# Kernel optimization log

Measured on AMD Instinct MI355X. Metric: run time of the kernel, lower is better.

Reference implementation:

```python
import jax, jax.numpy as jnp
import numpy as np

C = 128                  # stem_dim
CONV_DIM = C * C * 3 * 3 # 147456
B, T = 32, 30
N_CH = 1024
N_ANS = 32               # n_answers + 1
V = 44

UNARY = [4,10,11,12,13,14,15,16,17,18,19,20,21,22,23,24,25,29,30,31,32,33,34,35,36,37,38,39,40,41,43]
BINARY = [5,6,7,8,9,26,27,28,42]
SCENE_TOK = 4

_kind = np.zeros(V, np.int32)   # 0=special, 1=scene, 2=unary, 3=binary
_uidx = np.zeros(V, np.int32)
_bidx = np.zeros(V, np.int32)
for _j, _t in enumerate(UNARY):
    _kind[_t] = 2; _uidx[_t] = _j
for _j, _t in enumerate(BINARY):
    _kind[_t] = 3; _bidx[_t] = _j
_kind[SCENE_TOK] = 1
KIND_T, U_T, B_T = jnp.array(_kind), jnp.array(_uidx), jnp.array(_bidx)


def conv3x3(x, w):  # x [N,C,H,W], w [O,I,3,3], pad=1
    return jax.lax.conv_general_dilated(x, w, (1, 1), ((1, 1), (1, 1)),
                                        dimension_numbers=('NCHW', 'OIHW', 'NCHW'))


def conv1x1(x, w):
    return jax.lax.conv_general_dilated(x, w, (1, 1), ((0, 0), (0, 0)),
                                        dimension_numbers=('NCHW', 'OIHW', 'NCHW'))

# per-sample weights: vmap conv over batch
_bconv = jax.vmap(lambda x, w: conv3x3(x[None], w)[0])


def exec_unary(x, w1, w2):
    return jax.nn.relu(_bconv(jax.nn.relu(_bconv(x, w1)), w2))


def exec_binary(x1, x2, w1, w2, w3):
    h = jax.nn.relu(_bconv(jnp.concatenate([x1, x2], axis=1), w1))
    h = jax.nn.relu(_bconv(h, w2))
    return jax.nn.relu(_bconv(h, w3))


def setup_inputs() -> dict:
    key = jax.random.key(0)
    ks = jax.random.split(key, 10)
    std = 1.0 / float(np.sqrt(CONV_DIM))
    r = lambda k, shp, s: jax.random.normal(k, shp, jnp.float32) * s
    return {
        'feats': jax.random.normal(ks[0], (B, N_CH, 14, 14), jnp.float32),
        'programs': jax.random.randint(ks[1], (B, T), 0, V, dtype=jnp.int32),
        'stem_w1': r(ks[2], (C, N_CH, 3, 3), 0.02),
        'stem_b1': jnp.zeros((C,), jnp.float32),
        'stem_w2': r(ks[3], (C, C, 3, 3), 0.05),
        'stem_b2': jnp.zeros((C,), jnp.float32),
        'mem_u': jax.random.uniform(ks[4], (31, 2 * CONV_DIM), jnp.float32, -std, std),
        'mem_b': jax.random.uniform(ks[5], (9, 4 * CONV_DIM), jnp.float32, -std, std),
        'cls_w': r(ks[6], (512, C, 1, 1), 0.05),
        'cls_b': jnp.zeros((512,), jnp.float32),
        'fc1_w': r(ks[7], (1024, 512 * 7 * 7), 0.01),
        'fc1_b': jnp.zeros((1024,), jnp.float32),
        'fc2_w': r(ks[8], (N_ANS, 1024), 0.03),
        'fc2_b': jnp.zeros((N_ANS,), jnp.float32),
    }


def reference(feats, programs, stem_w1, stem_b1, stem_w2, stem_b2, mem_u, mem_b,
              cls_w, cls_b, fc1_w, fc1_b, fc2_w, fc2_b):
    # stem: conv3x3 -> relu -> conv3x3 -> relu
    h = jax.nn.relu(conv3x3(feats, stem_w1) + stem_b1[None, :, None, None])
    feat = jax.nn.relu(conv3x3(h, stem_w2) + stem_b2[None, :, None, None])  # [B,C,14,14]

    def step(carry, tok):  # tok [B] int32
        out, saved = carry
        kind = KIND_T[tok]                           # [B]
        uread = mem_u[U_T[tok]]                      # [B, 2*CONV_DIM] one-hot memory read
        w1 = uread[:, :CONV_DIM].reshape(-1, C, C, 3, 3)
        w2 = uread[:, CONV_DIM:].reshape(-1, C, C, 3, 3)
        bread = mem_b[B_T[tok]]                      # [B, 4*CONV_DIM]
        bw1 = bread[:, :2 * CONV_DIM].reshape(-1, C, 2 * C, 3, 3)
        bw2 = bread[:, 2 * CONV_DIM:3 * CONV_DIM].reshape(-1, C, C, 3, 3)
        bw3 = bread[:, 3 * CONV_DIM:].reshape(-1, C, C, 3, 3)
        is_scene = (kind == 1)[:, None, None, None]
        u_in = jnp.where(is_scene, feat, out)        # scene runs on stem features
        u_out = exec_unary(u_in, w1, w2)
        b_out = exec_binary(out, saved, bw1, bw2, bw3)
        k4 = kind[:, None, None, None]
        new_saved = jnp.where(is_scene, out, saved)  # scene saves current output
        new_out = jnp.where(k4 == 0, out, jnp.where(k4 == 3, b_out, u_out))
        return (new_out, new_saved), None

    toks_rev = programs[:, ::-1].T.astype(jnp.int32)  # [T,B] reversed program
    (out, _), _ = jax.lax.scan(step, (feat, jnp.zeros_like(feat)), toks_rev)

    # classifier: conv1x1 -> relu -> maxpool2 -> flatten -> fc -> relu -> fc
    h = jax.nn.relu(conv1x1(out, cls_w) + cls_b[None, :, None, None])
    h = jax.lax.reduce_window(h, -jnp.inf, jax.lax.max, (1, 1, 2, 2), (1, 1, 2, 2), 'VALID')
    h = h.reshape(h.shape[0], -1)                     # [B, 512*7*7]
    h = jax.nn.relu(h @ fc1_w.T + fc1_b)
    return h @ fc2_w.T + fc2_b                        # [B, N_ANS]
```

## Files before the change

### kernel.cpp

```cpp
#include <hip/hip_runtime.h>


#define NSTEP 30
#define CD 147456
#define P 196
#define FSZ 25088
#define LROW 18
#define LBUF (272*LROW)

typedef __attribute__((ext_vector_type(8))) short short8;
typedef __attribute__((ext_vector_type(16))) float f32x16;

__constant__ int KIND_TBL[44] = {
  0,0,0,0,1,3,3,3,3,3, 2,2,2,2,2,2,2,2,2,2,
  2,2,2,2,2,2,3,3,3,2, 2,2,2,2,2,2,2,2,2,2, 2,2,3,2};
__constant__ int MIDX_TBL[44] = {
  0,0,0,0,0,0,1,2,3,4, 1,2,3,4,5,6,7,8,9,10,
  11,12,13,14,15,16,5,6,7,17, 18,19,20,21,22,23,24,25,26,27, 28,29,8,30};

__device__ __forceinline__ uint32_t bf16_rne(float x) {
  uint32_t u = __float_as_uint(x);
  return (u + 0x7fffu + ((u >> 16) & 1u)) >> 16;
}
__device__ __forceinline__ uint32_t pack_hl(float x) {
  uint32_t h = bf16_rne(x);
  float rest = x - __uint_as_float(h << 16);
  uint32_t l = bf16_rne(rest);
  return (h << 16) | l;
}
__device__ __forceinline__ float ld_sc0(const float* p) {
  return __hip_atomic_load(p, __ATOMIC_RELAXED, __HIP_MEMORY_SCOPE_AGENT);
}
__device__ __forceinline__ void st_sc(float* p, float v) {
  __hip_atomic_store(p, v, __ATOMIC_RELAXED, __HIP_MEMORY_SCOPE_AGENT);
}

__device__ __forceinline__ void bbar(int* __restrict__ ctr, int target) {
  __syncthreads();
  if (threadIdx.x == 0) {
    __hip_atomic_fetch_add(ctr, 1, __ATOMIC_RELAXED, __HIP_MEMORY_SCOPE_AGENT);
    while (__hip_atomic_load(ctr, __ATOMIC_RELAXED, __HIP_MEMORY_SCOPE_AGENT) < target)
      __builtin_amdgcn_s_sleep(2);
  }
  __syncthreads();
}

__global__ void __launch_bounds__(256) repack_kernel(
    const float* __restrict__ sw1, const float* __restrict__ sw2,
    const float* __restrict__ mu, const float* __restrict__ mb,
    uint32_t* __restrict__ Wp)
{
  const int blk = blockIdx.x;
  const int C = blk / 9, tap = blk % 9;
  const float* src; int nic, lc;
  if (C < 64)       { src = sw1; nic = 1024; lc = C; }
  else if (C < 72)  { src = sw2; nic = 128;  lc = C - 64; }
  else if (C < 568) { int u = (C - 72) >> 4, r = (C - 72) & 15;
                      src = mu + (size_t)u * 2 * CD + (size_t)(r >> 3) * CD;
                      nic = 128; lc = r & 7; }
  else              { int j = (C - 568) >> 5, r = (C - 568) & 31;
                      const float* base = mb + (size_t)j * 4 * CD;
                      if (r < 16)      { src = base;                  nic = 256; lc = r; }
                      else if (r < 24) { src = base + 2 * (size_t)CD; nic = 128; lc = r - 16; }
                      else             { src = base + 3 * (size_t)CD; nic = 128; lc = r - 24; } }
  const int mt = threadIdx.x >> 6, lane = threadIdx.x & 63;
  const int oc = mt * 32 + (lane & 31);
  const int ic0 = lc * 16 + (lane >> 5) * 8;
  uint32_t hw[4], lw[4];
#pragma unroll
  for (int pr = 0; pr < 4; ++pr) {
    uint32_t hh[2], ll[2];
#pragma unroll
    for (int e = 0; e < 2; ++e) {
      float x = src[((size_t)oc * nic + (ic0 + pr * 2 + e)) * 9 + tap];
      uint32_t h = bf16_rne(x);
      float rest = x - __uint_as_float(h << 16);
      hh[e] = h; ll[e] = bf16_rne(rest);
    }
    hw[pr] = hh[0] | (hh[1] << 16);
    lw[pr] = ll[0] | (ll[1] << 16);
  }
  uint32_t* dstb = Wp + (size_t)blk * 2048;
  *(uint4*)(dstb + (mt * 2 + 0) * 256 + lane * 4) = make_uint4(hw[0], hw[1], hw[2], hw[3]);
  *(uint4*)(dstb + (mt * 2 + 1) * 256 + lane * 4) = make_uint4(lw[0], lw[1], lw[2], lw[3]);
}

union BU { uint32_t u[4]; uint4 v; short8 s8; };

__device__ __forceinline__ void load_wchunk(const uint32_t* __restrict__ wb,
                                            BU* wh, BU* wl) {
#pragma unroll
  for (int t = 0; t < 9; ++t) {
    wh[t].v = *(const uint4*)(wb + t * 2048);
    wl[t].v = *(const uint4*)(wb + t * 2048 + 256);
  }
}

__device__ __forceinline__ void mfma_chunk(const uint32_t* __restrict__ sb,
                                           int pwbase, const BU* wh, const BU* wl,
                                           f32x16& acc) {
  const int TAPOFF[9] = {0, 1, 2, 16, 17, 18, 32, 33, 34};
#pragma unroll
  for (int tap = 0; tap < 9; ++tap) {
    const int pw = pwbase + TAPOFF[tap] * LROW;
    uint2 q0 = *(const uint2*)(sb + pw);
    uint2 q1 = *(const uint2*)(sb + pw + 2);
    uint2 q2 = *(const uint2*)(sb + pw + 4);
    uint2 q3 = *(const uint2*)(sb + pw + 6);
    BU Bh, Bl;
    Bh.u[0] = __builtin_amdgcn_perm(q0.y, q0.x, 0x07060302u);
    Bh.u[1] = __builtin_amdgcn_perm(q1.y, q1.x, 0x07060302u);
    Bh.u[2] = __builtin_amdgcn_perm(q2.y, q2.x, 0x07060302u);
    Bh.u[3] = __builtin_amdgcn_perm(q3.y, q3.x, 0x07060302u);
    Bl.u[0] = __builtin_amdgcn_perm(q0.y, q0.x, 0x05040100u);
    Bl.u[1] = __builtin_amdgcn_perm(q1.y, q1.x, 0x05040100u);
    Bl.u[2] = __builtin_amdgcn_perm(q2.y, q2.x, 0x05040100u);
    Bl.u[3] = __builtin_amdgcn_perm(q3.y, q3.x, 0x05040100u);
    acc = __builtin_amdgcn_mfma_f32_32x32x16_bf16(wh[tap].s8, Bh.s8, acc, 0, 0, 0);
    acc = __builtin_amdgcn_mfma_f32_32x32x16_bf16(wh[tap].s8, Bl.s8, acc, 0, 0, 0);
    acc = __builtin_amdgcn_mfma_f32_32x32x16_bf16(wl[tap].s8, Bh.s8, acc, 0, 0, 0);
  }
}

template<int MODE>
__device__ __forceinline__ void stage_load(
    const float* __restrict__ in0A, const float* __restrict__ in0B,
    const float* __restrict__ in1A, const float* __restrict__ in1B,
    int split, int cn, int ic16, const int* imgoff, float* sv)
{
  if (MODE == 0) {
    const float* sA = in0A + (size_t)(cn * 16 + ic16) * P;
#pragma unroll
    for (int i = 0; i < 9; ++i) {
      int off = imgoff[i];
      sv[i] = (off >= 0) ? sA[off] : 0.f;
    }
  } else if (MODE == 1) {
    size_t o = (size_t)(cn * 16 + ic16) * P;
    const float* sA = in0A + o;
    const float* sB = in0B + o;
#pragma unroll
    for (int i = 0; i < 9; ++i) {
      int off = imgoff[i];
      sv[i] = (off >= 0) ? fmaxf(ld_sc0(sA + off) + ld_sc0(sB + off), 0.f) : 0.f;
    }
  } else {
    const float* sA; const float* sB;
    if (cn < split) {
      size_t o = (size_t)(cn * 16 + ic16) * P;
      sA = in0A + o; sB = in0B + o;
    } else {
      size_t o = (size_t)((cn - split) * 16 + ic16) * P;
      sA = in1A + o; sB = in1B + o;
    }
#pragma unroll
    for (int i = 0; i < 9; ++i) {
      int off = imgoff[i];
      sv[i] = (off >= 0) ? fmaxf(ld_sc0(sA + off) + ld_sc0(sB + off), 0.f) : 0.f;
    }
  }
}

template<int MODE>
__device__ __forceinline__ void conv_run(
    uint32_t sbuf[2][LBUF],
    const float* __restrict__ in0A, const float* __restrict__ in0B,
    const float* __restrict__ in1A, const float* __restrict__ in1B,
    int split, int cbeg, int n,
    int C0, int mt,
    const uint32_t* __restrict__ Wp, const float* __restrict__ bias,
    float* __restrict__ dst, float* __restrict__ dst2, float* __restrict__ zb,
    const int* imgoff)
{
  const int tid = threadIdx.x;
  const int w = tid >> 6, lane = tid & 63, l31 = lane & 31, kq = lane >> 5;
  const int ic16 = tid >> 5, pl = tid & 31;
  const int pwbase = (32 * w + l31) * LROW + kq * 8;
  const bool cw = (w < 7);
  const uint32_t* wbase = Wp + (size_t)C0 * 9 * 2048 + (mt * 2) * 256 + lane * 4;

  f32x16 acc;
#pragma unroll
  for (int i = 0; i < 16; ++i) acc[i] = 0.f;

  BU whA[9], wlA[9], whB[9], wlB[9];
  if (cw) load_wchunk(wbase + (size_t)cbeg * 9 * 2048, whA, wlA);
  {
    float sv[9];
    stage_load<MODE>(in0A, in0B, in1A, in1B, split, cbeg, ic16, imgoff, sv);
#pragma unroll
    for (int i = 0; i < 9; ++i) {
      int p = pl + 32 * i;
      if (p < 272) sbuf[0][p * LROW + ic16] = pack_hl(sv[i]);
    }
  }
  __syncthreads();

  int k = 0;
  while (true) {
    {
      const bool more = (k + 1 < n);
      float sv[9];
      if (more) {
        stage_load<MODE>(in0A, in0B, in1A, in1B, split, cbeg + k + 1, ic16, imgoff, sv);
        if (cw) load_wchunk(wbase + (size_t)(cbeg + k + 1) * 9 * 2048, whB, wlB);
      }
      if (cw) mfma_chunk(&sbuf[k & 1][0], pwbase, whA, wlA, acc);
      if (more) {
#pragma unroll
        for (int i = 0; i < 9; ++i) {
          int p = pl + 32 * i;
          if (p < 272) sbuf[(k + 1) & 1][p * LROW + ic16] = pack_hl(sv[i]);
        }
      }
      __syncthreads();
      if (++k >= n) break;
    }
    {
      const bool more = (k + 1 < n);
      float sv[9];
      if (more) {
        stage_load<MODE>(in0A, in0B, in1A, in1B, split, cbeg + k + 1, ic16, imgoff, sv);
        if (cw) load_wchunk(wbase + (size_t)(cbeg + k + 1) * 9 * 2048, whA, wlA);
      }
      if (cw) mfma_chunk(&sbuf[k & 1][0], pwbase, whB, wlB, acc);
      if (more) {
#pragma unroll
        for (int i = 0; i < 9; ++i) {
          int p = pl + 32 * i;
          if (p < 272) sbuf[(k + 1) & 1][p * LROW + ic16] = pack_hl(sv[i]);
        }
      }
      __syncthreads();
      if (++k >= n) break;
    }
  }

  if (cw) {
    const int ox = l31 & 15, oy = 2 * w + (l31 >> 4);
    if (ox < 14) {
#pragma unroll
      for (int reg = 0; reg < 16; ++reg) {
        int row = (reg & 3) + 8 * (reg >> 2) + 4 * kq;
        int oc = mt * 32 + row;
        float v = acc[reg];
        if (bias) v += bias[row];
        st_sc(dst + (size_t)oc * P + oy * 14 + ox, v);
        if (dst2) st_sc(dst2 + (size_t)oc * P + oy * 14 + ox, v);
        if (zb)   st_sc(zb   + (size_t)oc * P + oy * 14 + ox, 0.f);
      }
    }
  }
}

__global__ void __launch_bounds__(512, 1) persist_kernel(
    const float* __restrict__ feats, const int* __restrict__ progs,
    const float* __restrict__ sb1, const float* __restrict__ sb2,
    const uint32_t* __restrict__ Wp,
    float* __restrict__ featA, float* __restrict__ featB,
    float* __restrict__ outbA, float* __restrict__ outbB,
    float* __restrict__ savedA, float* __restrict__ savedB,
    float* __restrict__ h1A, float* __restrict__ h1B,
    float* __restrict__ h2A, float* __restrict__ h2B,
    int* __restrict__ ctr)
{
  __shared__ uint32_t s_act[2][LBUF];
  const int tid = threadIdx.x;
  const int b = blockIdx.x & 31;
  const int slice = blockIdx.x >> 5;
  const int mt = slice & 3;
  const int kh = slice >> 2;
  const size_t bo = (size_t)b * FSZ;
  int* myctr = ctr + b * 32;
  int phase = 0;

  float* featP  = kh ? featB  : featA;
  float* outbP  = kh ? outbB  : outbA;
  float* savedP = kh ? savedB : savedA;
  float* h1P    = kh ? h1B    : h1A;
  float* h2P    = kh ? h2B    : h2A;
  const float* bias1 = kh ? nullptr : sb1 + mt * 32;
  const float* bias2 = kh ? nullptr : sb2 + mt * 32;

  int imgoff[9];
#pragma unroll
  for (int i = 0; i < 9; ++i) {
    int p = (tid & 31) + 32 * i;
    int row = p >> 4, col = p & 15;
    imgoff[i] = (p < 272 && row >= 1 && row <= 14 && col >= 1 && col <= 14)
                ? (row - 1) * 14 + (col - 1) : -1;
  }

  conv_run<0>(s_act, feats + (size_t)b * 1024 * P, nullptr, nullptr, nullptr,
              1 << 28, kh * 32, 32, 0, mt, Wp, bias1,
              h1P + bo, nullptr, nullptr, imgoff);
  bbar(myctr, ++phase * 8);
  conv_run<1>(s_act, h1A + bo, h1B + bo, nullptr, nullptr, 1 << 28,
              kh * 4, 4, 64, mt, Wp, bias2,
              featP + bo, outbP + bo, savedP + bo, imgoff);
  bbar(myctr, ++phase * 8);

  for (int s = 0; s < NSTEP; ++s) {
    int tok = progs[b * NSTEP + (NSTEP - 1 - s)];
    int kind = KIND_TBL[tok], mi = MIDX_TBL[tok];
    if (kind == 0) continue;
    if (kind == 1) {
      const size_t so = bo + (size_t)mt * 32 * P;
      for (int i = tid; i < 32 * P; i += 512)
        st_sc(&savedP[so + i], ld_sc0(&outbP[so + i]));
      int C0 = 72 + mi * 16;
      conv_run<1>(s_act, featA + bo, featB + bo, nullptr, nullptr, 1 << 28,
                  kh * 4, 4, C0, mt, Wp, nullptr, h1P + bo, nullptr, nullptr, imgoff);
      bbar(myctr, ++phase * 8);
      conv_run<1>(s_act, h1A + bo, h1B + bo, nullptr, nullptr, 1 << 28,
                  kh * 4, 4, C0 + 8, mt, Wp, nullptr, outbP + bo, nullptr, nullptr, imgoff);
      bbar(myctr, ++phase * 8);
    } else if (kind == 2) {
      int C0 = 72 + mi * 16;
      conv_run<1>(s_act, outbA + bo, outbB + bo, nullptr, nullptr, 1 << 28,
                  kh * 4, 4, C0, mt, Wp, nullptr, h1P + bo, nullptr, nullptr, imgoff);
      bbar(myctr, ++phase * 8);
      conv_run<1>(s_act, h1A + bo, h1B + bo, nullptr, nullptr, 1 << 28,
                  kh * 4, 4, C0 + 8, mt, Wp, nullptr, outbP + bo, nullptr, nullptr, imgoff);
      bbar(myctr, ++phase * 8);
    } else {
      int C0 = 568 + mi * 32;
      conv_run<2>(s_act, outbA + bo, outbB + bo, savedA + bo, savedB + bo, 8,
                  kh * 8, 8, C0, mt, Wp, nullptr, h1P + bo, nullptr, nullptr, imgoff);
      bbar(myctr, ++phase * 8);
      conv_run<1>(s_act, h1A + bo, h1B + bo, nullptr, nullptr, 1 << 28,
                  kh * 4, 4, C0 + 16, mt, Wp, nullptr, h2P + bo, nullptr, nullptr, imgoff);
      bbar(myctr, ++phase * 8);
      conv_run<1>(s_act, h2A + bo, h2B + bo, nullptr, nullptr, 1 << 28,
                  kh * 4, 4, C0 + 24, mt, Wp, nullptr, outbP + bo, nullptr, nullptr, imgoff);
      bbar(myctr, ++phase * 8);
    }
  }
}

__global__ void __launch_bounds__(256) cls_pool_kernel(
    const float* __restrict__ xA, const float* __restrict__ xB,
    const float* __restrict__ Wc, const float* __restrict__ bc,
    float* __restrict__ hB)
{
  const int b = blockIdx.y, og = blockIdx.x;
  const int oc0 = og * 64;
  __shared__ float s[16 * P];
  const float* xbA = xA + (size_t)b * FSZ;
  const float* xbB = xB + (size_t)b * FSZ;
  const int tid = threadIdx.x;
  float acc[13][4];
#pragma unroll
  for (int k = 0; k < 13; ++k) { acc[k][0] = acc[k][1] = acc[k][2] = acc[k][3] = 0.f; }
  for (int c0 = 0; c0 < 128; c0 += 16) {
    __syncthreads();
    for (int i = tid; i < 16 * P; i += 256)
      s[i] = fmaxf(xbA[(size_t)c0 * P + i] + xbB[(size_t)c0 * P + i], 0.f);
    __syncthreads();
#pragma unroll
    for (int k = 0; k < 13; ++k) {
      const int idx = k * 256 + tid;
      if (idx < 64 * 49) {
        const int oc = oc0 + idx / 49, pp = idx % 49;
        const int py = pp / 7, px = pp % 7;
        const int b0 = 2 * py * 14 + 2 * px, b1 = b0 + 14;
        const float* wr = Wc + (size_t)oc * 128 + c0;
#pragma unroll
        for (int ic = 0; ic < 16; ++ic) {
          const float w = wr[ic];
          const float* sp = s + ic * P;
          const float2 r0 = *(const float2*)(sp + b0);
          const float2 r1 = *(const float2*)(sp + b1);
          acc[k][0] = fmaf(w, r0.x, acc[k][0]);
          acc[k][1] = fmaf(w, r0.y, acc[k][1]);
          acc[k][2] = fmaf(w, r1.x, acc[k][2]);
          acc[k][3] = fmaf(w, r1.y, acc[k][3]);
        }
      }
    }
  }
#pragma unroll
  for (int k = 0; k < 13; ++k) {
    const int idx = k * 256 + tid;
    if (idx < 64 * 49) {
      const int oc = oc0 + idx / 49, pp = idx % 49;
      const float m = fmaxf(fmaxf(acc[k][0], acc[k][1]), fmaxf(acc[k][2], acc[k][3]));
      hB[(size_t)b * 25088 + (size_t)oc * 49 + pp] = fmaxf(m + bc[oc], 0.f);
    }
  }
}

__global__ void __launch_bounds__(256) transpose_kernel(
    const float* __restrict__ hB, float* __restrict__ hT)
{
  __shared__ float t[256 * 33];
  const int k0 = blockIdx.x * 256;
  const int tid = threadIdx.x;
  for (int b = 0; b < 32; ++b)
    t[tid * 33 + b] = hB[(size_t)b * 25088 + k0 + tid];
  __syncthreads();
  for (int i = tid; i < 256 * 32; i += 256) {
    const int k = i >> 5, b = i & 31;
    hT[(size_t)(k0 + k) * 32 + b] = t[k * 33 + b];
  }
}

__global__ void __launch_bounds__(256) fc1_kernel(
    const float* __restrict__ hT, const float* __restrict__ W,
    const float* __restrict__ bias, float* __restrict__ o)
{
  const int b = threadIdx.x & 31, j = threadIdx.x >> 5;
  const int oc = blockIdx.x * 4 + (j & 3);
  const int kh = j >> 2;
  const float* wr = W + (size_t)oc * 25088 + (size_t)kh * 12544;
  const float* ht = hT + (size_t)kh * 12544 * 32;
  float acc = 0.f;
  for (int k = 0; k < 12544; k += 4) {
    const float4 w4 = *(const float4*)(wr + k);
    acc = fmaf(ht[(size_t)(k + 0) * 32 + b], w4.x, acc);
    acc = fmaf(ht[(size_t)(k + 1) * 32 + b], w4.y, acc);
    acc = fmaf(ht[(size_t)(k + 2) * 32 + b], w4.z, acc);
    acc = fmaf(ht[(size_t)(k + 3) * 32 + b], w4.w, acc);
  }
  __shared__ float red[8][32];
  red[j][b] = acc;
  __syncthreads();
  if (j < 4)
    o[(size_t)b * 1024 + oc] = fmaxf(red[j][b] + red[j + 4][b] + bias[oc], 0.f);
}

__global__ void __launch_bounds__(256) fc2_kernel(
    const float* __restrict__ h, const float* __restrict__ W,
    const float* __restrict__ bias, float* __restrict__ out)
{
  const int i = blockIdx.x * 256 + threadIdx.x;
  const int b = i >> 5, oo = i & 31;
  const float* wr = W + (size_t)oo * 1024;
  const float* hr = h + (size_t)b * 1024;
  float acc = bias[oo];
  for (int k = 0; k < 1024; k += 4) {
    const float4 w4 = *(const float4*)(wr + k);
    const float4 h4 = *(const float4*)(hr + k);
    acc = fmaf(h4.x, w4.x, acc);
    acc = fmaf(h4.y, w4.y, acc);
    acc = fmaf(h4.z, w4.z, acc);
    acc = fmaf(h4.w, w4.w, acc);
  }
  out[i] = acc;
}

extern "C" void kernel_launch(void* const* d_in, const int* in_sizes, int n_in,
                              void* d_out, int out_size, void* d_ws, size_t ws_size,
                              hipStream_t stream) {
  const float* feats   = (const float*)d_in[0];
  const int*   progs   = (const int*)  d_in[1];
  const float* stem_w1 = (const float*)d_in[2];
  const float* stem_b1 = (const float*)d_in[3];
  const float* stem_w2 = (const float*)d_in[4];
  const float* stem_b2 = (const float*)d_in[5];
  const float* mem_u   = (const float*)d_in[6];
  const float* mem_b   = (const float*)d_in[7];
  const float* cls_w   = (const float*)d_in[8];
  const float* cls_b   = (const float*)d_in[9];
  const float* fc1_w   = (const float*)d_in[10];
  const float* fc1_b   = (const float*)d_in[11];
  const float* fc2_w   = (const float*)d_in[12];
  const float* fc2_b   = (const float*)d_in[13];

  float* ws = (float*)d_ws;
  const size_t F = (size_t)32 * FSZ;
  float*    featA  = ws + 0 * F;
  float*    featB  = ws + 1 * F;
  float*    outbA  = ws + 2 * F;
  float*    outbB  = ws + 3 * F;
  float*    savedA = ws + 4 * F;
  float*    savedB = ws + 5 * F;
  float*    h1A    = ws + 6 * F;
  float*    h1B    = ws + 7 * F;
  float*    h2A    = ws + 8 * F;
  float*    h2B    = ws + 9 * F;
  uint32_t* Wp    = (uint32_t*)(ws + 10 * F);
  int*      ctr   = (int*)(Wp + (size_t)7704 * 2048);

  hipMemsetAsync(ctr, 0, 32 * 32 * sizeof(int), stream);

  repack_kernel<<<dim3(7704), dim3(256), 0, stream>>>(stem_w1, stem_w2, mem_u, mem_b, Wp);

  persist_kernel<<<dim3(256), dim3(512), 0, stream>>>(
      feats, progs, stem_b1, stem_b2, Wp,
      featA, featB, outbA, outbB, savedA, savedB, h1A, h1B, h2A, h2B, ctr);

  float* hB   = h1A;
  float* hT   = h2A;
  float* fc1o = savedA;
  cls_pool_kernel<<<dim3(8, 32), dim3(256), 0, stream>>>(outbA, outbB, cls_w, cls_b, hB);
  transpose_kernel<<<dim3(98), dim3(256), 0, stream>>>(hB, hT);
  fc1_kernel<<<dim3(256), dim3(256), 0, stream>>>(hT, fc1_w, fc1_b, fc1o);
  fc2_kernel<<<dim3(4), dim3(256), 0, stream>>>(fc1o, fc2_w, fc2_b, (float*)d_out);
}
```

Baseline: 2.945 ms.

## Stage four input-channel chunks per LDS round to cut conv barriers

The conv loop now stages four 16-channel activation chunks into a four-slot LDS buffer per group. This replaces the earlier two-slot ping-pong that synced after every chunk, so there is one barrier pair per four chunks instead of one barrier per chunk. Weight loads stay double-buffered in registers per chunk. The binary first conv is simplified by mapping each kh half directly to outb or saved. The occupancy hint changes to amdgpu_waves_per_eu(2,2), and the larger sv arrays and LDS footprint add register and LDS pressure.

```diff
diff --git a/kernel.cpp b/kernel.cpp
--- a/kernel.cpp
+++ b/kernel.cpp
@@ -124,54 +124,49 @@
 
 template<int MODE>
 __device__ __forceinline__ void stage_load(
-    const float* __restrict__ in0A, const float* __restrict__ in0B,
-    const float* __restrict__ in1A, const float* __restrict__ in1B,
-    int split, int cn, int ic16, const int* imgoff, float* sv)
+    const float* __restrict__ inA, const float* __restrict__ inB,
+    int cn, int ic16, const int* imgoff, float* sv)
 {
   if (MODE == 0) {
-    const float* sA = in0A + (size_t)(cn * 16 + ic16) * P;
+    const float* sA = inA + (size_t)(cn * 16 + ic16) * P;
 #pragma unroll
     for (int i = 0; i < 9; ++i) {
       int off = imgoff[i];
       sv[i] = (off >= 0) ? sA[off] : 0.f;
     }
-  } else if (MODE == 1) {
+  } else {
     size_t o = (size_t)(cn * 16 + ic16) * P;
-    const float* sA = in0A + o;
-    const float* sB = in0B + o;
+    const float* sA = inA + o;
+    const float* sB = inB + o;
 #pragma unroll
     for (int i = 0; i < 9; ++i) {
       int off = imgoff[i];
       sv[i] = (off >= 0) ? fmaxf(ld_sc0(sA + off) + ld_sc0(sB + off), 0.f) : 0.f;
     }
-  } else {
-    const float* sA; const float* sB;
-    if (cn < split) {
-      size_t o = (size_t)(cn * 16 + ic16) * P;
-      sA = in0A + o; sB = in0B + o;
-    } else {
-      size_t o = (size_t)((cn - split) * 16 + ic16) * P;
-      sA = in1A + o; sB = in1B + o;
-    }
-#pragma unroll
-    for (int i = 0; i < 9; ++i) {
-      int off = imgoff[i];
-      sv[i] = (off >= 0) ? fmaxf(ld_sc0(sA + off) + ld_sc0(sB + off), 0.f) : 0.f;
-    }
-  }
-}
-
-template<int MODE>
+  }
+}
+
+__device__ __forceinline__ void lds_write_chunk(uint32_t* __restrict__ sb,
+                                                int pl, int ic16, const float* sv) {
+#pragma unroll
+  for (int i = 0; i < 9; ++i) {
+    int p = pl + 32 * i;
+    if (p < 272) sb[p * LROW + ic16] = pack_hl(sv[i]);
+  }
+}
+
+template<int MODE, int N>
 __device__ __forceinline__ void conv_run(
-    uint32_t sbuf[2][LBUF],
-    const float* __restrict__ in0A, const float* __restrict__ in0B,
-    const float* __restrict__ in1A, const float* __restrict__ in1B,
-    int split, int cbeg, int n,
+    uint32_t (*sbuf)[LBUF],
+    const float* __restrict__ inA, const float* __restrict__ inB,
+    int cbeg, int wbeg,
     int C0, int mt,
     const uint32_t* __restrict__ Wp, const float* __restrict__ bias,
     float* __restrict__ dst, float* __restrict__ dst2, float* __restrict__ zb,
     const int* imgoff)
 {
+  static_assert(N % 4 == 0, "N must be a multiple of 4");
+  constexpr int NG = N / 4;
   const int tid = threadIdx.x;
   const int w = tid >> 6, lane = tid & 63, l31 = lane & 31, kq = lane >> 5;
   const int ic16 = tid >> 5, pl = tid & 31;
@@ -184,55 +179,45 @@
   for (int i = 0; i < 16; ++i) acc[i] = 0.f;
 
   BU whA[9], wlA[9], whB[9], wlB[9];
-  if (cw) load_wchunk(wbase + (size_t)cbeg * 9 * 2048, whA, wlA);
-  {
-    float sv[9];
-    stage_load<MODE>(in0A, in0B, in1A, in1B, split, cbeg, ic16, imgoff, sv);
-#pragma unroll
-    for (int i = 0; i < 9; ++i) {
-      int p = pl + 32 * i;
-      if (p < 272) sbuf[0][p * LROW + ic16] = pack_hl(sv[i]);
-    }
-  }
+  if (cw) load_wchunk(wbase + (size_t)wbeg * 9 * 2048, whA, wlA);
+
+  float sv[4][9];
+#pragma unroll
+  for (int t = 0; t < 4; ++t)
+    stage_load<MODE>(inA, inB, cbeg + t, ic16, imgoff, sv[t]);
+#pragma unroll
+  for (int t = 0; t < 4; ++t)
+    lds_write_chunk(&sbuf[t][0], pl, ic16, sv[t]);
   __syncthreads();
 
-  int k = 0;
-  while (true) {
-    {
-      const bool more = (k + 1 < n);
-      float sv[9];
-      if (more) {
-        stage_load<MODE>(in0A, in0B, in1A, in1B, split, cbeg + k + 1, ic16, imgoff, sv);
-        if (cw) load_wchunk(wbase + (size_t)(cbeg + k + 1) * 9 * 2048, whB, wlB);
-      }
-      if (cw) mfma_chunk(&sbuf[k & 1][0], pwbase, whA, wlA, acc);
-      if (more) {
-#pragma unroll
-        for (int i = 0; i < 9; ++i) {
-          int p = pl + 32 * i;
-          if (p < 272) sbuf[(k + 1) & 1][p * LROW + ic16] = pack_hl(sv[i]);
+#pragma unroll
+  for (int g = 0; g < NG; ++g) {
+    if (g + 1 < NG) {
+#pragma unroll
+      for (int t = 0; t < 4; ++t)
+        stage_load<MODE>(inA, inB, cbeg + (g + 1) * 4 + t, ic16, imgoff, sv[t]);
+    }
+#pragma unroll
+    for (int t = 0; t < 4; ++t) {
+      const int c = g * 4 + t;
+      if (cw) {
+        if ((t & 1) == 0) {
+          if (c + 1 < N)
+            load_wchunk(wbase + (size_t)(wbeg + c + 1) * 9 * 2048, whB, wlB);
+          mfma_chunk(&sbuf[t][0], pwbase, whA, wlA, acc);
+        } else {
+          if (c + 1 < N)
+            load_wchunk(wbase + (size_t)(wbeg + c + 1) * 9 * 2048, whA, wlA);
+          mfma_chunk(&sbuf[t][0], pwbase, whB, wlB, acc);
         }
       }
+    }
+    if (g + 1 < NG) {
       __syncthreads();
-      if (++k >= n) break;
-    }
-    {
-      const bool more = (k + 1 < n);
-      float sv[9];
-      if (more) {
-        stage_load<MODE>(in0A, in0B, in1A, in1B, split, cbeg + k + 1, ic16, imgoff, sv);
-        if (cw) load_wchunk(wbase + (size_t)(cbeg + k + 1) * 9 * 2048, whA, wlA);
-      }
-      if (cw) mfma_chunk(&sbuf[k & 1][0], pwbase, whB, wlB, acc);
-      if (more) {
-#pragma unroll
-        for (int i = 0; i < 9; ++i) {
-          int p = pl + 32 * i;
-          if (p < 272) sbuf[(k + 1) & 1][p * LROW + ic16] = pack_hl(sv[i]);
-        }
-      }
+#pragma unroll
+      for (int t = 0; t < 4; ++t)
+        lds_write_chunk(&sbuf[t][0], pl, ic16, sv[t]);
       __syncthreads();
-      if (++k >= n) break;
     }
   }
 
@@ -253,7 +238,8 @@
   }
 }
 
-__global__ void __launch_bounds__(512, 1) persist_kernel(
+__attribute__((amdgpu_waves_per_eu(2, 2)))
+__global__ void __launch_bounds__(512) persist_kernel(
     const float* __restrict__ feats, const int* __restrict__ progs,
     const float* __restrict__ sb1, const float* __restrict__ sb2,
     const uint32_t* __restrict__ Wp,
@@ -264,7 +250,7 @@
     float* __restrict__ h2A, float* __restrict__ h2B,
     int* __restrict__ ctr)
 {
-  __shared__ uint32_t s_act[2][LBUF];
+  __shared__ uint32_t s_act[4][LBUF];
   const int tid = threadIdx.x;
   const int b = blockIdx.x & 31;
   const int slice = blockIdx.x >> 5;
@@ -291,13 +277,12 @@
                 ? (row - 1) * 14 + (col - 1) : -1;
   }
 
-  conv_run<0>(s_act, feats + (size_t)b * 1024 * P, nullptr, nullptr, nullptr,
-              1 << 28, kh * 32, 32, 0, mt, Wp, bias1,
-              h1P + bo, nullptr, nullptr, imgoff);
+  conv_run<0, 32>(s_act, feats + (size_t)b * 1024 * P, nullptr,
+                  kh * 32, kh * 32, 0, mt, Wp, bias1,
+                  h1P + bo, nullptr, nullptr, imgoff);
   bbar(myctr, ++phase * 8);
-  conv_run<1>(s_act, h1A + bo, h1B + bo, nullptr, nullptr, 1 << 28,
-              kh * 4, 4, 64, mt, Wp, bias2,
-              featP + bo, outbP + bo, savedP + bo, imgoff);
+  conv_run<1, 4>(s_act, h1A + bo, h1B + bo, kh * 4, kh * 4, 64, mt, Wp, bias2,
+                 featP + bo, outbP + bo, savedP + bo, imgoff);
   bbar(myctr, ++phase * 8);
 
   for (int s = 0; s < NSTEP; ++s) {
@@ -309,30 +294,32 @@
       for (int i = tid; i < 32 * P; i += 512)
         st_sc(&savedP[so + i], ld_sc0(&outbP[so + i]));
       int C0 = 72 + mi * 16;
-      conv_run<1>(s_act, featA + bo, featB + bo, nullptr, nullptr, 1 << 28,
-                  kh * 4, 4, C0, mt, Wp, nullptr, h1P + bo, nullptr, nullptr, imgoff);
-      bbar(myctr, ++phase * 8);
-      conv_run<1>(s_act, h1A + bo, h1B + bo, nullptr, nullptr, 1 << 28,
-                  kh * 4, 4, C0 + 8, mt, Wp, nullptr, outbP + bo, nullptr, nullptr, imgoff);
+      conv_run<1, 4>(s_act, featA + bo, featB + bo, kh * 4, kh * 4, C0, mt, Wp,
+                     nullptr, h1P + bo, nullptr, nullptr, imgoff);
+      bbar(myctr, ++phase * 8);
+      conv_run<1, 4>(s_act, h1A + bo, h1B + bo, kh * 4, kh * 4, C0 + 8, mt, Wp,
+                     nullptr, outbP + bo, nullptr, nullptr, imgoff);
       bbar(myctr, ++phase * 8);
     } else if (kind == 2) {
       int C0 = 72 + mi * 16;
-      conv_run<1>(s_act, outbA + bo, outbB + bo, nullptr, nullptr, 1 << 28,
-                  kh * 4, 4, C0, mt, Wp, nullptr, h1P + bo, nullptr, nullptr, imgoff);
-      bbar(myctr, ++phase * 8);
-      conv_run<1>(s_act, h1A + bo, h1B + bo, nullptr, nullptr, 1 << 28,
-                  kh * 4, 4, C0 + 8, mt, Wp, nullptr, outbP + bo, nullptr, nullptr, imgoff);
+      conv_run<1, 4>(s_act, outbA + bo, outbB + bo, kh * 4, kh * 4, C0, mt, Wp,
+                     nullptr, h1P + bo, nullptr, nullptr, imgoff);
+      bbar(myctr, ++phase * 8);
+      conv_run<1, 4>(s_act, h1A + bo, h1B + bo, kh * 4, kh * 4, C0 + 8, mt, Wp,
+                     nullptr, outbP + bo, nullptr, nullptr, imgoff);
       bbar(myctr, ++phase * 8);
     } else {
       int C0 = 568 + mi * 32;
-      conv_run<2>(s_act, outbA + bo, outbB + bo, savedA + bo, savedB + bo, 8,
-                  kh * 8, 8, C0, mt, Wp, nullptr, h1P + bo, nullptr, nullptr, imgoff);
-      bbar(myctr, ++phase * 8);
-      conv_run<1>(s_act, h1A + bo, h1B + bo, nullptr, nullptr, 1 << 28,
-                  kh * 4, 4, C0 + 16, mt, Wp, nullptr, h2P + bo, nullptr, nullptr, imgoff);
-      bbar(myctr, ++phase * 8);
-      conv_run<1>(s_act, h2A + bo, h2B + bo, nullptr, nullptr, 1 << 28,
-                  kh * 4, 4, C0 + 24, mt, Wp, nullptr, outbP + bo, nullptr, nullptr, imgoff);
+      conv_run<1, 8>(s_act, kh ? savedA + bo : outbA + bo,
+                     kh ? savedB + bo : outbB + bo,
+                     0, kh * 8, C0, mt, Wp,
+                     nullptr, h1P + bo, nullptr, nullptr, imgoff);
+      bbar(myctr, ++phase * 8);
+      conv_run<1, 4>(s_act, h1A + bo, h1B + bo, kh * 4, kh * 4, C0 + 16, mt, Wp,
+                     nullptr, h2P + bo, nullptr, nullptr, imgoff);
+      bbar(myctr, ++phase * 8);
+      conv_run<1, 4>(s_act, h2A + bo, h2B + bo, kh * 4, kh * 4, C0 + 24, mt, Wp,
+                     nullptr, outbP + bo, nullptr, nullptr, imgoff);
       bbar(myctr, ++phase * 8);
     }
   }
```

New measurement: 5.364 ms. +82.1%, slower.
